# Optimization experiments

Hardware: AMD Instinct MI355X
Metric: run time of the kernel (lower is better)

Reference implementation:

```python
import jax, jax.numpy as jnp
import numpy as np

RES = 512
MAX_DEPTH = 100.0
AMBIENT = 0.3
LIGHT_STREN = 0.8
SHININESS = 16.0
EPS = 1e-8


def _unit(v):
    return v / (jnp.linalg.norm(v, axis=-1, keepdims=True) + EPS)


def setup_inputs() -> dict:
    key = jax.random.key(0)
    ks = jax.random.split(key, 8)
    B, N, M, TEX = 1, 512, 128, 512
    verts = jax.random.uniform(ks[0], (B, N, 3), minval=-1.0, maxval=1.0, dtype=jnp.float32)
    faces = jax.random.randint(ks[1], (B, M, 3), 0, N, dtype=jnp.int32)
    normals = jax.random.normal(ks[2], (B, M, 3, 3), dtype=jnp.float32)
    uvs = jax.random.uniform(ks[3], (B, M, 3, 2), dtype=jnp.float32)
    textures = jax.random.uniform(ks[4], (B, TEX, TEX, 3), dtype=jnp.float32)
    f = RES / 2.0
    K = jnp.array([[f, 0.0, RES / 2.0], [0.0, f, RES / 2.0], [0.0, 0.0, 1.0]], jnp.float32)
    Ks = jnp.broadcast_to(K, (B, 3, 3))
    RT = jnp.concatenate([jnp.eye(3, dtype=jnp.float32), jnp.array([[0.0], [0.0], [2.0]], jnp.float32)], axis=1)
    RTs = jnp.broadcast_to(RT, (B, 3, 4))
    view_dir = jax.random.normal(ks[5], (B, 3), dtype=jnp.float32)
    light_dir = jax.random.normal(ks[6], (B, 3), dtype=jnp.float32)
    return {"verts": verts, "faces": faces, "normals": normals, "uvs": uvs,
            "textures": textures, "Ks": Ks, "RTs": RTs, "view_dir": view_dir, "light_dir": light_dir}


def _render(verts, faces, normals, uvs, textures, Ks, RTs, view_dir, light_dir):
    B = verts.shape[0]
    # camera space: cam = R @ v + t
    cam = jnp.einsum('bij,bnj->bni', RTs[:, :, :3], verts) + RTs[:, None, :, 3]
    # orthographic projection to pixel coords
    x = Ks[:, None, 0, 0] * cam[..., 0] + Ks[:, None, 0, 2]
    y = Ks[:, None, 1, 1] * cam[..., 1] + Ks[:, None, 1, 2]
    xy = jnp.stack([x, y], -1)            # [B,N,2]
    z = cam[..., 2]                        # [B,N]
    gather_v = jax.vmap(lambda a, f: a[f])
    tv = gather_v(xy, faces)               # [B,M,3,2] screen-space triangle corners
    tz = gather_v(z, faces)                # [B,M,3]
    # pixel centers, row-major (p = row*RES + col)
    ii = jnp.arange(RES, dtype=jnp.float32) + 0.5
    py, px = jnp.meshgrid(ii, ii, indexing='ij')
    pix = jnp.stack([px.ravel(), py.ravel()], -1)   # [P,2]

    def edge(a, b, p):
        return (b[..., 0] - a[..., 0]) * (p[..., 1] - a[..., 1]) - (b[..., 1] - a[..., 1]) * (p[..., 0] - a[..., 0])

    v0, v1, v2 = tv[:, None, :, 0], tv[:, None, :, 1], tv[:, None, :, 2]  # [B,1,M,2]
    p = pix[None, :, None]                                               # [1,P,1,2]
    w0 = edge(v1, v2, p)                   # [B,P,M]
    w1 = edge(v2, v0, p)
    w2 = edge(v0, v1, p)
    area = w0 + w1 + w2
    inside = (((w0 >= 0) & (w1 >= 0) & (w2 >= 0)) | ((w0 <= 0) & (w1 <= 0) & (w2 <= 0))) & (jnp.abs(area) > EPS)
    inv_a = 1.0 / jnp.where(jnp.abs(area) > EPS, area, 1.0)
    zpix = (w0 * tz[:, None, :, 0] + w1 * tz[:, None, :, 1] + w2 * tz[:, None, :, 2]) * inv_a
    valid = inside & (zpix > 0)
    zc = jnp.where(valid, zpix, MAX_DEPTH)   # [B,P,M] candidate depths
    depth = jnp.min(zc, axis=-1)             # z-buffer result [B,P]
    win = jnp.argmin(zc, axis=-1)             # winning triangle per pixel [B,P]
    hit = depth < MAX_DEPTH

    # recompute barycentrics for the winning triangle only (avoids [B,P,M,3])
    gpick = jax.vmap(lambda a, i: a[i])
    tvw = gpick(tv, win)                      # [B,P,3,2]
    nw = gpick(normals, win)                  # [B,P,3,3]
    uvw = gpick(uvs, win)                     # [B,P,3,2]
    pp = pix[None]                            # [1,P,2]

    def e2(a, b):
        return (b[..., 0] - a[..., 0]) * (pp[..., 1] - a[..., 1]) - (b[..., 1] - a[..., 1]) * (pp[..., 0] - a[..., 0])

    u0 = e2(tvw[:, :, 1], tvw[:, :, 2])
    u1 = e2(tvw[:, :, 2], tvw[:, :, 0])
    u2 = e2(tvw[:, :, 0], tvw[:, :, 1])
    ar = u0 + u1 + u2
    inv2 = 1.0 / jnp.where(jnp.abs(ar) > EPS, ar, 1.0)
    bary = jnp.stack([u0, u1, u2], -1) * inv2[..., None]   # [B,P,3]
    nrm = _unit(jnp.einsum('bpk,bpkc->bpc', bary, nw))     # interpolated normal
    uv = jnp.einsum('bpk,bpkc->bpc', bary, uvw)            # interpolated uv [B,P,2]

    # bilinear texture sampling
    Ht, Wt = textures.shape[1], textures.shape[2]
    uu = jnp.clip(uv[..., 0], 0.0, 1.0) * (Wt - 1)
    vv = jnp.clip(uv[..., 1], 0.0, 1.0) * (Ht - 1)
    x0 = jnp.floor(uu).astype(jnp.int32)
    y0 = jnp.floor(vv).astype(jnp.int32)
    x1 = jnp.minimum(x0 + 1, Wt - 1)
    y1 = jnp.minimum(y0 + 1, Ht - 1)
    fx = (uu - x0.astype(jnp.float32))[..., None]
    fy = (vv - y0.astype(jnp.float32))[..., None]
    tget = jax.vmap(lambda t, a, b: t[a, b])
    col = (tget(textures, y0, x0) * (1 - fx) * (1 - fy) + tget(textures, y0, x1) * fx * (1 - fy)
           + tget(textures, y1, x0) * (1 - fx) * fy + tget(textures, y1, x1) * fx * fy)  # [B,P,3]

    # Lambert diffuse + Blinn-Phong specular
    ld = _unit(light_dir)
    vd = _unit(view_dir)
    diff = jnp.clip(jnp.einsum('bpc,bc->bp', nrm, ld), 0.0)
    h = _unit(ld + vd)
    spec = LIGHT_STREN * jnp.clip(jnp.einsum('bpc,bc->bp', nrm, h), 0.0) ** SHININESS
    shade = col * (AMBIENT + LIGHT_STREN * diff)[..., None] + spec[..., None]
    rgb = jnp.where(hit[..., None], shade, 0.0)

    depths = depth.reshape(B, RES, RES)
    rgbs = rgb.reshape(B, RES, RES, 3)
    masks = hit.reshape(B, RES, RES).astype(jnp.int32)
    return depths, rgbs, masks


def reference(verts, faces, normals, uvs, textures, Ks, RTs, view_dir, light_dir):
    return _render(verts, faces, normals, uvs, textures, Ks, RTs, view_dir, light_dir)
```

## Files before the change

kernel.cpp:

```cpp
#include <hip/hip_runtime.h>
#include <math.h>

#pragma clang fp contract(off)

#define RES         512
#define TILE        16
#define TILESX      (RES / TILE)
#define MAXF        128
#define MAX_DEPTH   100.0f
#define AMBIENT     0.3f
#define LIGHT_STREN 0.8f
#define EPSF        1e-8f
#define MARG        1.0f

__global__ __launch_bounds__(256) void mesh_render_tiled(
    const float* __restrict__ verts,
    const int*   __restrict__ faces,
    const float* __restrict__ normals,
    const float* __restrict__ uvs,
    const float* __restrict__ tex,
    const float* __restrict__ Ks,
    const float* __restrict__ RTs,
    const float* __restrict__ view_dir,
    const float* __restrict__ light_dir,
    float* __restrict__ out,
    int M, int TEXW, int TEXH)
{
    __shared__ float cfd[MAXF][16];
    __shared__ int   cid[MAXF];
    __shared__ unsigned long long smask[2];
    __shared__ float slit[6];

    const int tid = threadIdx.x;
    const int tx  = blockIdx.x % TILESX;
    const int ty  = blockIdx.x / TILESX;
    const float PX0 = (float)(tx * TILE) + 0.5f;
    const float PY0 = (float)(ty * TILE) + 0.5f;

    bool flag = false;
    float e0dx=0,e0dy=0,e0ax=0,e0ay=0, e1dx=0,e1dy=0,e1ax=0,e1ay=0;
    float e2dx=0,e2dy=0,e2ax=0,e2ay=0, Z0=0,Z1=0,Z2=0;
    unsigned long long mymask = 0;

    if (tid < MAXF) {
        if (tid < M) {
            const float r00 = RTs[0], r01 = RTs[1], r02 = RTs[2],  t0 = RTs[3];
            const float r10 = RTs[4], r11 = RTs[5], r12 = RTs[6],  t1 = RTs[7];
            const float r20 = RTs[8], r21 = RTs[9], r22 = RTs[10], t2 = RTs[11];
            const float k00 = Ks[0], k02 = Ks[2], k11 = Ks[4], k12 = Ks[5];
            float X[3], Y[3], Z[3];
            #pragma unroll
            for (int k = 0; k < 3; ++k) {
                int vi = faces[tid * 3 + k];
                float vx = verts[vi * 3 + 0];
                float vy = verts[vi * 3 + 1];
                float vz = verts[vi * 3 + 2];
                float cx = ((r00 * vx + r01 * vy) + r02 * vz) + t0;
                float cy = ((r10 * vx + r11 * vy) + r12 * vz) + t1;
                float cz = ((r20 * vx + r21 * vy) + r22 * vz) + t2;
                X[k] = k00 * cx + k02;
                Y[k] = k11 * cy + k12;
                Z[k] = cz;
            }
            e0dx = X[2]-X[1]; e0dy = Y[2]-Y[1]; e0ax = X[1]; e0ay = Y[1];
            e1dx = X[0]-X[2]; e1dy = Y[0]-Y[2]; e1ax = X[2]; e1ay = Y[2];
            e2dx = X[1]-X[0]; e2dy = Y[1]-Y[0]; e2ax = X[0]; e2ay = Y[0];
            Z0 = Z[0]; Z1 = Z[1]; Z2 = Z[2];

            float minX = fminf(fminf(X[0],X[1]),X[2]);
            float maxX = fmaxf(fmaxf(X[0],X[1]),X[2]);
            float minY = fminf(fminf(Y[0],Y[1]),Y[2]);
            float maxY = fmaxf(fmaxf(Y[0],Y[1]),Y[2]);
            bool bb = (minX <= PX0 + 15.0f + MARG) && (maxX >= PX0 - MARG) &&
                      (minY <= PY0 + 15.0f + MARG) && (maxY >= PY0 - MARG);

            float wA0 = e0dx*(PY0-e0ay) - e0dy*(PX0-e0ax);
            float wA1 = e1dx*(PY0-e1ay) - e1dy*(PX0-e1ax);
            float wA2 = e2dx*(PY0-e2ay) - e2dy*(PX0-e2ax);
            float area = (wA0 + wA1) + wA2;
            float amin = fminf(area, 0.0f) - MARG, amax = fmaxf(area, 0.0f) + MARG;

            float s0x = -e0dy*15.0f, s0y = e0dx*15.0f;
            float s1x = -e1dy*15.0f, s1y = e1dx*15.0f;
            float s2x = -e2dy*15.0f, s2y = e2dx*15.0f;
            float t0min = wA0 + fminf(s0x,0.f) + fminf(s0y,0.f);
            float t0max = wA0 + fmaxf(s0x,0.f) + fmaxf(s0y,0.f);
            float t1min = wA1 + fminf(s1x,0.f) + fminf(s1y,0.f);
            float t1max = wA1 + fmaxf(s1x,0.f) + fmaxf(s1y,0.f);
            float t2min = wA2 + fminf(s2x,0.f) + fminf(s2y,0.f);
            float t2max = wA2 + fmaxf(s2x,0.f) + fmaxf(s2y,0.f);
            bool ok0 = (t0max >= amin) && (t0min <= amax);
            bool ok1 = (t1max >= amin) && (t1min <= amax);
            bool ok2 = (t2max >= amin) && (t2min <= amax);
            flag = bb && ok0 && ok1 && ok2;
        }
        mymask = __ballot(flag);
        if ((tid & 63) == 0) smask[tid >> 6] = mymask;
    }
    if (tid == 128) {
        float lx = light_dir[0], ly = light_dir[1], lz = light_dir[2];
        float ll = sqrtf((lx*lx + ly*ly) + lz*lz) + 1e-8f;
        lx /= ll; ly /= ll; lz /= ll;
        float vx = view_dir[0], vy = view_dir[1], vz = view_dir[2];
        float vl = sqrtf((vx*vx + vy*vy) + vz*vz) + 1e-8f;
        vx /= vl; vy /= vl; vz /= vl;
        float hx = lx + vx, hy = ly + vy, hz = lz + vz;
        float hl = sqrtf((hx*hx + hy*hy) + hz*hz) + 1e-8f;
        slit[0] = lx; slit[1] = ly; slit[2] = lz;
        slit[3] = hx / hl; slit[4] = hy / hl; slit[5] = hz / hl;
    }
    __syncthreads();

    if (flag) {
        int base = (tid >= 64) ? __popcll(smask[0]) : 0;
        int pos  = base + __popcll(mymask & ((1ull << (tid & 63)) - 1ull));
        float* dd = cfd[pos];
        dd[0]=e0dx; dd[1]=e0dy; dd[2]=e0ax; dd[3]=e0ay;
        dd[4]=e1dx; dd[5]=e1dy; dd[6]=e1ax; dd[7]=e1ay;
        dd[8]=e2dx; dd[9]=e2dy; dd[10]=e2ax; dd[11]=e2ay;
        dd[12]=Z0;  dd[13]=Z1;  dd[14]=Z2;  dd[15]=0.0f;
        cid[pos] = tid;
    }
    __syncthreads();
    const int cnt = __popcll(smask[0]) + __popcll(smask[1]);

    const int lx_ = tid & (TILE-1), ly_ = tid / TILE;
    const float px = PX0 + (float)lx_;
    const float py = PY0 + (float)ly_;
    const int p = (ty*TILE + ly_) * RES + (tx*TILE + lx_);

    float best = MAX_DEPTH;
    int winpos = -1;
    for (int i = 0; i < cnt; ++i) {
        const float4 q0 = *reinterpret_cast<const float4*>(&cfd[i][0]);
        const float4 q1 = *reinterpret_cast<const float4*>(&cfd[i][4]);
        const float4 q2 = *reinterpret_cast<const float4*>(&cfd[i][8]);
        const float4 q3 = *reinterpret_cast<const float4*>(&cfd[i][12]);
        float w0 = q0.x * (py - q0.w) - q0.y * (px - q0.z);
        float w1 = q1.x * (py - q1.w) - q1.y * (px - q1.z);
        float w2 = q2.x * (py - q2.w) - q2.y * (px - q2.z);
        float area = (w0 + w1) + w2;
        bool nz = fabsf(area) > EPSF;
        bool inside = (((w0 >= 0.0f) && (w1 >= 0.0f) && (w2 >= 0.0f)) ||
                       ((w0 <= 0.0f) && (w1 <= 0.0f) && (w2 <= 0.0f))) && nz;
        float inva = __builtin_amdgcn_rcpf(nz ? area : 1.0f);
        float zpix = ((w0 * q3.x + w1 * q3.y) + w2 * q3.z) * inva;
        float zc = (inside && (zpix > 0.0f)) ? zpix : MAX_DEPTH;
        if (zc < best) { best = zc; winpos = i; }
    }

    float r = 0.0f, g = 0.0f, b = 0.0f, mk = 0.0f, depth = MAX_DEPTH;
    if (winpos >= 0) {
        mk = 1.0f;
        depth = best;
        const int f = cid[winpos];
        const float* d = cfd[winpos];
        float u0 = d[0] * (py - d[3])  - d[1] * (px - d[2]);
        float u1 = d[4] * (py - d[7])  - d[5] * (px - d[6]);
        float u2 = d[8] * (py - d[11]) - d[9] * (px - d[10]);
        float ar = (u0 + u1) + u2;
        float inv2 = __builtin_amdgcn_rcpf((fabsf(ar) > EPSF) ? ar : 1.0f);
        float b0 = u0 * inv2, b1 = u1 * inv2, b2 = u2 * inv2;

        const float* nw = normals + f * 9;
        float nx  = (b0 * nw[0] + b1 * nw[3]) + b2 * nw[6];
        float ny  = (b0 * nw[1] + b1 * nw[4]) + b2 * nw[7];
        float nzv = (b0 * nw[2] + b1 * nw[5]) + b2 * nw[8];
        float nl  = __builtin_amdgcn_sqrtf((nx*nx + ny*ny) + nzv*nzv) + 1e-8f;
        float rn  = __builtin_amdgcn_rcpf(nl);
        nx *= rn; ny *= rn; nzv *= rn;

        const float* uvp = uvs + f * 6;
        float uvx = (b0 * uvp[0] + b1 * uvp[2]) + b2 * uvp[4];
        float uvy = (b0 * uvp[1] + b1 * uvp[3]) + b2 * uvp[5];
        float uu = fminf(fmaxf(uvx, 0.0f), 1.0f) * (float)(TEXW - 1);
        float vv = fminf(fmaxf(uvy, 0.0f), 1.0f) * (float)(TEXH - 1);
        int x0 = (int)floorf(uu), y0 = (int)floorf(vv);
        int x1 = min(x0 + 1, TEXW - 1), y1 = min(y0 + 1, TEXH - 1);
        float fx = uu - (float)x0, fy = vv - (float)y0;
        const float* t00 = tex + (y0 * TEXW + x0) * 3;
        const float* t01 = tex + (y0 * TEXW + x1) * 3;
        const float* t10 = tex + (y1 * TEXW + x0) * 3;
        const float* t11 = tex + (y1 * TEXW + x1) * 3;
        float gx = 1.0f - fx, gy = 1.0f - fy;
        float cr = (((t00[0]*gx)*gy + (t01[0]*fx)*gy) + (t10[0]*gx)*fy) + (t11[0]*fx)*fy;
        float cg = (((t00[1]*gx)*gy + (t01[1]*fx)*gy) + (t10[1]*gx)*fy) + (t11[1]*fx)*fy;
        float cb = (((t00[2]*gx)*gy + (t01[2]*fx)*gy) + (t10[2]*gx)*fy) + (t11[2]*fx)*fy;

        float ldx = slit[0], ldy = slit[1], ldz = slit[2];
        float hx  = slit[3], hy  = slit[4], hz  = slit[5];
        float diff = fmaxf((nx*ldx + ny*ldy) + nzv*ldz, 0.0f);
        float sd   = fmaxf((nx*hx  + ny*hy)  + nzv*hz,  0.0f);
        float s2 = sd*sd, s4 = s2*s2, s8 = s4*s4, s16 = s8*s8;
        float spec  = LIGHT_STREN * s16;
        float scale = AMBIENT + LIGHT_STREN * diff;
        r = cr * scale + spec;
        g = cg * scale + spec;
        b = cb * scale + spec;
    }

    out[p] = depth;
    float* rgb = out + RES * RES;
    rgb[3 * p + 0] = r;
    rgb[3 * p + 1] = g;
    rgb[3 * p + 2] = b;
    out[RES * RES * 4 + p] = mk;
}

extern "C" void kernel_launch(void* const* d_in, const int* in_sizes, int n_in,
                              void* d_out, int out_size, void* d_ws, size_t ws_size,
                              hipStream_t stream) {
    const float* verts     = (const float*)d_in[0];
    const int*   faces     = (const int*)  d_in[1];
    const float* normals   = (const float*)d_in[2];
    const float* uvs       = (const float*)d_in[3];
    const float* tex       = (const float*)d_in[4];
    const float* Ks        = (const float*)d_in[5];
    const float* RTs       = (const float*)d_in[6];
    const float* view_dir  = (const float*)d_in[7];
    const float* light_dir = (const float*)d_in[8];

    int M = in_sizes[1] / 3;
    if (M > MAXF) M = MAXF;
    const int texels = in_sizes[4] / 3;
    const int TEXW = (int)(sqrt((double)texels) + 0.5);
    const int TEXH = TEXW;

    const int blocks = TILESX * TILESX;
    mesh_render_tiled<<<blocks, 256, 0, stream>>>(
        verts, faces, normals, uvs, tex, Ks, RTs, view_dir, light_dir,
        (float*)d_out, M, TEXW, TEXH);
}
```

Measured before the change: 18.54 us.

## Bucket faces by min depth and skip occluded faces per wavefront

Compacted per-tile face lists are now ordered into 8 coarse buckets by minimum vertex depth, and each face stores its min depth minus a guard. The raster loop skips a face when every lane's current best depth is already at or below that bound, so later far faces cost one LDS read. The winning face's barycentric weights are kept from the loop instead of recomputed, and the inside test uses min/max. The risks are extra ballot and prefix work per block, and tie-breaking order changing because faces are no longer in index order, which could alter which face wins on equal depth.

Result: faster. 15.68 us, median of 2 (-15.4%).

```diff
diff --git a/kernel.cpp b/kernel.cpp
--- a/kernel.cpp
+++ b/kernel.cpp
@@ -12,6 +12,7 @@
 #define LIGHT_STREN 0.8f
 #define EPSF        1e-8f
 #define MARG        1.0f
+#define ZGUARD      1e-3f
 
 __global__ __launch_bounds__(256) void mesh_render_tiled(
     const float* __restrict__ verts,
@@ -28,7 +29,7 @@
 {
     __shared__ float cfd[MAXF][16];
     __shared__ int   cid[MAXF];
-    __shared__ unsigned long long smask[2];
+    __shared__ int   scnt[2][8];
     __shared__ float slit[6];
 
     const int tid = threadIdx.x;
@@ -38,9 +39,10 @@
     const float PY0 = (float)(ty * TILE) + 0.5f;
 
     bool flag = false;
+    int  bkt  = -1;
     float e0dx=0,e0dy=0,e0ax=0,e0ay=0, e1dx=0,e1dy=0,e1ax=0,e1ay=0;
-    float e2dx=0,e2dy=0,e2ax=0,e2ay=0, Z0=0,Z1=0,Z2=0;
-    unsigned long long mymask = 0;
+    float e2dx=0,e2dy=0,e2ax=0,e2ay=0, Z0=0,Z1=0,Z2=0, MZ=0;
+    unsigned long long bmask = 0;
 
     if (tid < MAXF) {
         if (tid < M) {
@@ -66,6 +68,7 @@
             e1dx = X[0]-X[2]; e1dy = Y[0]-Y[2]; e1ax = X[2]; e1ay = Y[2];
             e2dx = X[1]-X[0]; e2dy = Y[1]-Y[0]; e2ax = X[0]; e2ay = Y[0];
             Z0 = Z[0]; Z1 = Z[1]; Z2 = Z[2];
+            MZ = fminf(fminf(Z0, Z1), Z2);
 
             float minX = fminf(fminf(X[0],X[1]),X[2]);
             float maxX = fmaxf(fmaxf(X[0],X[1]),X[2]);
@@ -93,9 +96,17 @@
             bool ok1 = (t1max >= amin) && (t1min <= amax);
             bool ok2 = (t2max >= amin) && (t2min <= amax);
             flag = bb && ok0 && ok1 && ok2;
+            if (flag) {
+                int bq = (int)((MZ - 1.0f) * 4.0f);
+                bkt = bq < 0 ? 0 : (bq > 7 ? 7 : bq);
+            }
         }
-        mymask = __ballot(flag);
-        if ((tid & 63) == 0) smask[tid >> 6] = mymask;
+        #pragma unroll
+        for (int k = 0; k < 8; ++k) {
+            unsigned long long mk = __ballot(flag && (bkt == k));
+            if (bkt == k) bmask = mk;
+            if ((tid & 63) == 0) scnt[tid >> 6][k] = __popcll(mk);
+        }
     }
     if (tid == 128) {
         float lx = light_dir[0], ly = light_dir[1], lz = light_dir[2];
@@ -112,17 +123,22 @@
     __syncthreads();
 
     if (flag) {
-        int base = (tid >= 64) ? __popcll(smask[0]) : 0;
-        int pos  = base + __popcll(mymask & ((1ull << (tid & 63)) - 1ull));
+        int wv = tid >> 6;
+        int base = 0;
+        for (int k = 0; k < bkt; ++k) base += scnt[0][k] + scnt[1][k];
+        if (wv == 1) base += scnt[0][bkt];
+        int pos = base + __popcll(bmask & ((1ull << (tid & 63)) - 1ull));
         float* dd = cfd[pos];
         dd[0]=e0dx; dd[1]=e0dy; dd[2]=e0ax; dd[3]=e0ay;
         dd[4]=e1dx; dd[5]=e1dy; dd[6]=e1ax; dd[7]=e1ay;
         dd[8]=e2dx; dd[9]=e2dy; dd[10]=e2ax; dd[11]=e2ay;
-        dd[12]=Z0;  dd[13]=Z1;  dd[14]=Z2;  dd[15]=0.0f;
+        dd[12]=Z0;  dd[13]=Z1;  dd[14]=Z2;  dd[15]=MZ - ZGUARD;
         cid[pos] = tid;
     }
     __syncthreads();
-    const int cnt = __popcll(smask[0]) + __popcll(smask[1]);
+    int cnt = 0;
+    #pragma unroll
+    for (int k = 0; k < 8; ++k) cnt += scnt[0][k] + scnt[1][k];
 
     const int lx_ = tid & (TILE-1), ly_ = tid / TILE;
     const float px = PX0 + (float)lx_;
@@ -130,23 +146,29 @@
     const int p = (ty*TILE + ly_) * RES + (tx*TILE + lx_);
 
     float best = MAX_DEPTH;
+    float w0s = 0.0f, w1s = 0.0f, w2s = 0.0f, invs = 1.0f;
     int winpos = -1;
     for (int i = 0; i < cnt; ++i) {
+        const float4 q3 = *reinterpret_cast<const float4*>(&cfd[i][12]);
+        if (__all(q3.w >= best)) continue;
         const float4 q0 = *reinterpret_cast<const float4*>(&cfd[i][0]);
         const float4 q1 = *reinterpret_cast<const float4*>(&cfd[i][4]);
         const float4 q2 = *reinterpret_cast<const float4*>(&cfd[i][8]);
-        const float4 q3 = *reinterpret_cast<const float4*>(&cfd[i][12]);
         float w0 = q0.x * (py - q0.w) - q0.y * (px - q0.z);
         float w1 = q1.x * (py - q1.w) - q1.y * (px - q1.z);
         float w2 = q2.x * (py - q2.w) - q2.y * (px - q2.z);
         float area = (w0 + w1) + w2;
+        float mn = fminf(fminf(w0, w1), w2);
+        float mx = fmaxf(fmaxf(w0, w1), w2);
         bool nz = fabsf(area) > EPSF;
-        bool inside = (((w0 >= 0.0f) && (w1 >= 0.0f) && (w2 >= 0.0f)) ||
-                       ((w0 <= 0.0f) && (w1 <= 0.0f) && (w2 <= 0.0f))) && nz;
+        bool inside = ((mn >= 0.0f) || (mx <= 0.0f)) && nz;
         float inva = __builtin_amdgcn_rcpf(nz ? area : 1.0f);
         float zpix = ((w0 * q3.x + w1 * q3.y) + w2 * q3.z) * inva;
         float zc = (inside && (zpix > 0.0f)) ? zpix : MAX_DEPTH;
-        if (zc < best) { best = zc; winpos = i; }
+        if (zc < best) {
+            best = zc; winpos = i;
+            w0s = w0; w1s = w1; w2s = w2; invs = inva;
+        }
     }
 
     float r = 0.0f, g = 0.0f, b = 0.0f, mk = 0.0f, depth = MAX_DEPTH;
@@ -154,13 +176,7 @@
         mk = 1.0f;
         depth = best;
         const int f = cid[winpos];
-        const float* d = cfd[winpos];
-        float u0 = d[0] * (py - d[3])  - d[1] * (px - d[2]);
-        float u1 = d[4] * (py - d[7])  - d[5] * (px - d[6]);
-        float u2 = d[8] * (py - d[11]) - d[9] * (px - d[10]);
-        float ar = (u0 + u1) + u2;
-        float inv2 = __builtin_amdgcn_rcpf((fabsf(ar) > EPSF) ? ar : 1.0f);
-        float b0 = u0 * inv2, b1 = u1 * inv2, b2 = u2 * inv2;
+        float b0 = w0s * invs, b1 = w1s * invs, b2 = w2s * invs;
 
         const float* nw = normals + f * 9;
         float nx  = (b0 * nw[0] + b1 * nw[3]) + b2 * nw[6];
```
